# Kernel optimization log

Measured on AMD Instinct MI355X. Metric: run time of the kernel, lower is better.

Reference implementation:

```python
import jax, jax.numpy as jnp
import numpy as np

WAVE_LEN = 1000.0
DIM_G = 64


def box_relational_embedding(boxes):
    # boxes: (B, N, 4) -> (B, N, N, 64) trigonometric geometry embedding
    B, N, _ = boxes.shape
    x_min, y_min, x_max, y_max = jnp.split(boxes, 4, axis=-1)  # each (B,N,1)
    cx = (x_min + x_max) * 0.5
    cy = (y_min + y_max) * 0.5
    w = (x_max - x_min) + 1.0
    h = (y_max - y_min) + 1.0
    cxT = jnp.swapaxes(cx, 1, 2)  # (B,1,N)
    cyT = jnp.swapaxes(cy, 1, 2)
    dx = jnp.log(jnp.clip(jnp.abs((cx - cxT) / w), 1e-3))  # (B,N,N)
    dy = jnp.log(jnp.clip(jnp.abs((cy - cyT) / h), 1e-3))
    dw = jnp.log(w / jnp.swapaxes(w, 1, 2))
    dh = jnp.log(h / jnp.swapaxes(h, 1, 2))
    pos = jnp.stack([dx, dy, dw, dh], axis=-1)  # (B,N,N,4)
    n_freq = DIM_G // 8  # 8 frequency bands
    dim_mat = 1.0 / (WAVE_LEN ** (jnp.arange(n_freq, dtype=pos.dtype) / n_freq))
    mul = (100.0 * pos)[..., None] * dim_mat  # (B,N,N,4,8)
    mul = mul.reshape(B, N, N, 4 * n_freq)  # (B,N,N,32)
    return jnp.concatenate([jnp.sin(mul), jnp.cos(mul)], axis=-1)  # (B,N,N,64)


def setup_inputs() -> dict:
    key = jax.random.key(0)
    ks = jax.random.split(key, 12)
    B, N, D, H = 32, 196, 1024, 8
    scale = 0.02
    inp = {
        "input_query": jax.random.normal(ks[0], (B, N, D), jnp.float32),
        "input_key": jax.random.normal(ks[1], (B, N, D), jnp.float32),
        "input_value": jax.random.normal(ks[2], (B, N, D), jnp.float32),
        "input_box": jax.random.uniform(ks[3], (B, N, 4), jnp.float32),
        "Wq": jax.random.normal(ks[4], (D, D), jnp.float32) * scale,
        "bq": jnp.zeros((D,), jnp.float32),
        "Wk": jax.random.normal(ks[5], (D, D), jnp.float32) * scale,
        "bk": jnp.zeros((D,), jnp.float32),
        "Wv": jax.random.normal(ks[6], (D, D), jnp.float32) * scale,
        "bv": jnp.zeros((D,), jnp.float32),
        "Wo": jax.random.normal(ks[7], (D, D), jnp.float32) * scale,
        "bo": jnp.zeros((D,), jnp.float32),
        "WG_w": jax.random.normal(ks[8], (H, DIM_G), jnp.float32) * scale,  # 8 stacked (64->1) linears
        "WG_b": jnp.zeros((H,), jnp.float32),
    }
    return inp


def reference(input_query, input_key, input_value, input_box,
              Wq, bq, Wk, bk, Wv, bv, Wo, bo, WG_w, WG_b):
    B, N, D = input_query.shape
    H = WG_w.shape[0]
    dk = D // H
    # relation geometry weights per head: (B,H,N,N)
    geo = box_relational_embedding(input_box)  # (B,N,N,64)
    wg = jax.nn.relu(jnp.einsum('bnmg,hg->bhnm', geo, WG_w) + WG_b[None, :, None, None])
    # projections (torch Linear: x @ W.T + b), reshape to (B,H,N,dk)
    def proj(x, W, b):
        return (x @ W.T + b).reshape(B, N, H, dk).transpose(0, 2, 1, 3)
    q = proj(input_query, Wq, bq)
    k = proj(input_key, Wk, bk)
    v = proj(input_value, Wv, bv)
    scores = jnp.einsum('bhnd,bhmd->bhnm', q, k) / np.sqrt(dk).astype(q.dtype)
    logits = jnp.log(jnp.clip(wg, 1e-6)) + scores
    attn = jax.nn.softmax(logits, axis=-1)  # (B,H,N,N)
    out = jnp.einsum('bhnm,bhmd->bhnd', attn, v)  # (B,H,N,dk)
    out = out.transpose(0, 2, 1, 3).reshape(B, N, D)
    return out @ Wo.T + bo
```

## Files before the change

kernel.cpp:

```cpp
#include <hip/hip_runtime.h>
#include <hip/hip_bf16.h>

typedef __bf16 bf16;
typedef _Float16 half_t;
typedef bf16 bf16x8 __attribute__((ext_vector_type(8)));
typedef bf16 bf16x4 __attribute__((ext_vector_type(4)));
typedef float floatx4 __attribute__((ext_vector_type(4)));

#define B_ 32
#define N_ 196
#define H_ 8
#define D_ 1024
#define DK_ 128
#define BN_ (B_ * N_)
#define BH_ (B_ * H_)
#define NPAD_ 224
#define PSTRIDE_ 232

typedef __attribute__((address_space(3))) unsigned int lds_uint;
typedef const __attribute__((address_space(1))) unsigned int glb_uint;

__device__ __forceinline__ void async_copy16(const bf16* g, bf16* l) {
  __builtin_amdgcn_global_load_lds((glb_uint*)g, (lds_uint*)l, 16, 0, 0);
}

__device__ __forceinline__ bf16x8 bzero8() {
  bf16x8 z;
#pragma unroll
  for (int i = 0; i < 8; i++) z[i] = (bf16)0.0f;
  return z;
}

__global__ __launch_bounds__(256) void cvt3_kernel(const float* __restrict__ s0,
                                                   const float* __restrict__ s1,
                                                   const float* __restrict__ s2,
                                                   bf16* __restrict__ d0,
                                                   bf16* __restrict__ d1,
                                                   bf16* __restrict__ d2, int n4) {
  const int which = blockIdx.y;
  const float* s = (which == 0) ? s0 : (which == 1) ? s1 : s2;
  bf16* d = (which == 0) ? d0 : (which == 1) ? d1 : d2;
  int i = blockIdx.x * 256 + threadIdx.x;
  if (i >= n4) return;
  float4 v = ((const float4*)s)[i];
  bf16x4 o;
  o[0] = (bf16)v.x;
  o[1] = (bf16)v.y;
  o[2] = (bf16)v.z;
  o[3] = (bf16)v.w;
  *(bf16x4*)(d + (size_t)i * 4) = o;
}

__global__ __launch_bounds__(256) void cvt4_kernel(const float* __restrict__ s0,
                                                   const float* __restrict__ s1,
                                                   const float* __restrict__ s2,
                                                   const float* __restrict__ s3,
                                                   bf16* __restrict__ d0,
                                                   bf16* __restrict__ d1,
                                                   bf16* __restrict__ d2,
                                                   bf16* __restrict__ d3, int n4) {
  const int which = blockIdx.y;
  const float* s = (which == 0) ? s0 : (which == 1) ? s1 : (which == 2) ? s2 : s3;
  bf16* d = (which == 0) ? d0 : (which == 1) ? d1 : (which == 2) ? d2 : d3;
  int i = blockIdx.x * 256 + threadIdx.x;
  if (i >= n4) return;
  float4 v = ((const float4*)s)[i];
  bf16x4 o;
  o[0] = (bf16)v.x;
  o[1] = (bf16)v.y;
  o[2] = (bf16)v.z;
  o[3] = (bf16)v.w;
  *(bf16x4*)(d + (size_t)i * 4) = o;
}

__global__ __launch_bounds__(256) void geo_kernel(const float* __restrict__ box,
                                                  const float* __restrict__ WGw,
                                                  const float* __restrict__ WGb,
                                                  half_t* __restrict__ S) {
  __shared__ float4 wsh[128];
  if (threadIdx.x < 128) wsh[threadIdx.x] = ((const float4*)WGw)[threadIdx.x];
  __syncthreads();

  int tid = blockIdx.x * 256 + threadIdx.x;
  int b = tid / (N_ * N_);
  int rem = tid - b * (N_ * N_);
  int n = rem / N_;
  int m = rem - n * N_;

  float4 bn = ((const float4*)box)[b * N_ + n];
  float4 bm = ((const float4*)box)[b * N_ + m];
  float cxn = (bn.x + bn.z) * 0.5f, cyn = (bn.y + bn.w) * 0.5f;
  float wn = bn.z - bn.x + 1.0f, hn = bn.w - bn.y + 1.0f;
  float cxm = (bm.x + bm.z) * 0.5f, cym = (bm.y + bm.w) * 0.5f;
  float wm = bm.z - bm.x + 1.0f, hm = bm.w - bm.y + 1.0f;

  float pos[4];
  pos[0] = __logf(fmaxf(fabsf((cxn - cxm) / wn), 1e-3f));
  pos[1] = __logf(fmaxf(fabsf((cyn - cym) / hn), 1e-3f));
  pos[2] = __logf(wn / wm);
  pos[3] = __logf(hn / hm);

  const float dims[8] = {1.0f,          0.4216965034f, 0.1778279410f, 0.0749894209f,
                         0.0316227766f, 0.0133352143f, 0.0056234133f, 0.0023713737f};
  float feat[64];
#pragma unroll
  for (int p = 0; p < 4; p++) {
#pragma unroll
    for (int f = 0; f < 8; f++) {
      float a = 100.0f * pos[p] * dims[f];
      feat[p * 8 + f] = __sinf(a);
      feat[32 + p * 8 + f] = __cosf(a);
    }
  }
#pragma unroll
  for (int hh = 0; hh < 8; hh++) {
    float accv = WGb[hh];
#pragma unroll
    for (int g4 = 0; g4 < 16; g4++) {
      float4 wv = wsh[hh * 16 + g4];
      accv += feat[g4 * 4 + 0] * wv.x + feat[g4 * 4 + 1] * wv.y +
              feat[g4 * 4 + 2] * wv.z + feat[g4 * 4 + 3] * wv.w;
    }
    S[((size_t)((b * H_ + hh) * N_ + n)) * NPAD_ + m] = (half_t)fmaxf(accv, 1e-6f);
  }
}

template <int MODE>
__global__ __launch_bounds__(256) void gemm_nt(const bf16* __restrict__ A,
                                               const bf16* __restrict__ W,
                                               const float* __restrict__ bias,
                                               void* __restrict__ Cout, int M, int K,
                                               int Nd) {
  __shared__ bf16 As[128 * 32];
  __shared__ bf16 Bs[128 * 32];

  const int wave = threadIdx.x >> 6;
  const int lane = threadIdx.x & 63;
  const int l16 = lane & 15;
  const int quad = lane >> 4;

  const bf16* gA = A + (size_t)blockIdx.x * 128 * K;
  const bf16* gB = W + (size_t)blockIdx.y * 128 * K;

  const int srow = lane >> 2;
  const int scol = (lane & 3) * 8;
  const int seg0 = wave * 2;
  const size_t gOffA0 = (size_t)(seg0 * 16 + srow) * K + scol;
  const size_t gOffA1 = (size_t)(seg0 * 16 + 16 + srow) * K + scol;
  bf16* lA0 = As + seg0 * 512 + lane * 8;
  bf16* lA1 = As + (seg0 + 1) * 512 + lane * 8;
  bf16* lB0 = Bs + seg0 * 512 + lane * 8;
  bf16* lB1 = Bs + (seg0 + 1) * 512 + lane * 8;

  floatx4 acc[4][4];
#pragma unroll
  for (int i = 0; i < 4; i++)
#pragma unroll
    for (int j = 0; j < 4; j++)
#pragma unroll
      for (int r = 0; r < 4; r++) acc[i][j][r] = 0.0f;

  async_copy16(gA + gOffA0, lA0);
  async_copy16(gA + gOffA1, lA1);
  async_copy16(gB + gOffA0, lB0);
  async_copy16(gB + gOffA1, lB1);

  const bf16* rA = As + ((wave >> 1) * 64 + l16) * 32 + quad * 8;
  const bf16* rB = Bs + ((wave & 1) * 64 + l16) * 32 + quad * 8;

  for (int k0 = 0; k0 < K; k0 += 32) {
    __syncthreads();
    bf16x8 af[4], bfv[4];
#pragma unroll
    for (int i = 0; i < 4; i++) af[i] = *(const bf16x8*)(rA + i * 16 * 32);
#pragma unroll
    for (int j = 0; j < 4; j++) bfv[j] = *(const bf16x8*)(rB + j * 16 * 32);
    __syncthreads();
    if (k0 + 32 < K) {
      const bf16* gAn = gA + k0 + 32;
      const bf16* gBn = gB + k0 + 32;
      async_copy16(gAn + gOffA0, lA0);
      async_copy16(gAn + gOffA1, lA1);
      async_copy16(gBn + gOffA0, lB0);
      async_copy16(gBn + gOffA1, lB1);
    }
#pragma unroll
    for (int i = 0; i < 4; i++)
#pragma unroll
      for (int j = 0; j < 4; j++)
        acc[i][j] = __builtin_amdgcn_mfma_f32_16x16x32_bf16(af[i], bfv[j], acc[i][j], 0, 0, 0);
  }

  const int m0 = blockIdx.x * 128 + (wave >> 1) * 64;
  const int n0 = blockIdx.y * 128 + (wave & 1) * 64;
#pragma unroll
  for (int j = 0; j < 4; j++) {
    const int col = n0 + j * 16 + l16;
    const float bv = bias[col];
#pragma unroll
    for (int i = 0; i < 4; i++) {
#pragma unroll
      for (int r = 0; r < 4; r++) {
        const int row = m0 + i * 16 + quad * 4 + r;
        float v = acc[i][j][r] + bv;
        if (MODE == 0) {
          ((bf16*)Cout)[(size_t)row * Nd + col] = (bf16)v;
        } else if (MODE == 1) {
          ((float*)Cout)[(size_t)row * Nd + col] = v;
        } else {
          int b = row / N_;
          int n = row - b * N_;
          int h = col >> 7;
          int d = col & (DK_ - 1);
          ((bf16*)Cout)[((size_t)((b * H_ + h) * DK_ + d)) * NPAD_ + n] = (bf16)v;
        }
      }
    }
  }
}

__global__ __launch_bounds__(256) void gemm_qkv(
    const bf16* __restrict__ Aq, const bf16* __restrict__ Ak, const bf16* __restrict__ Av,
    const bf16* __restrict__ Wq, const bf16* __restrict__ Wk, const bf16* __restrict__ Wv,
    const float* __restrict__ bq, const float* __restrict__ bk, const float* __restrict__ bv,
    bf16* __restrict__ Oq, bf16* __restrict__ Ok, bf16* __restrict__ Vt) {
  const int z = blockIdx.z;
  const bf16* A = (z == 0) ? Aq : (z == 1) ? Ak : Av;
  const bf16* W = (z == 0) ? Wq : (z == 1) ? Wk : Wv;
  const float* bias = (z == 0) ? bq : (z == 1) ? bk : bv;
  constexpr int K = D_;

  __shared__ bf16 As[128 * 32];
  __shared__ bf16 Bs[128 * 32];

  const int wave = threadIdx.x >> 6;
  const int lane = threadIdx.x & 63;
  const int l16 = lane & 15;
  const int quad = lane >> 4;

  const bf16* gA = A + (size_t)blockIdx.x * 128 * K;
  const bf16* gB = W + (size_t)blockIdx.y * 128 * K;

  const int srow = lane >> 2;
  const int scol = (lane & 3) * 8;
  const int seg0 = wave * 2;
  const size_t gOffA0 = (size_t)(seg0 * 16 + srow) * K + scol;
  const size_t gOffA1 = (size_t)(seg0 * 16 + 16 + srow) * K + scol;
  bf16* lA0 = As + seg0 * 512 + lane * 8;
  bf16* lA1 = As + (seg0 + 1) * 512 + lane * 8;
  bf16* lB0 = Bs + seg0 * 512 + lane * 8;
  bf16* lB1 = Bs + (seg0 + 1) * 512 + lane * 8;

  floatx4 acc[4][4];
#pragma unroll
  for (int i = 0; i < 4; i++)
#pragma unroll
    for (int j = 0; j < 4; j++)
#pragma unroll
      for (int r = 0; r < 4; r++) acc[i][j][r] = 0.0f;

  async_copy16(gA + gOffA0, lA0);
  async_copy16(gA + gOffA1, lA1);
  async_copy16(gB + gOffA0, lB0);
  async_copy16(gB + gOffA1, lB1);

  const bf16* rA = As + ((wave >> 1) * 64 + l16) * 32 + quad * 8;
  const bf16* rB = Bs + ((wave & 1) * 64 + l16) * 32 + quad * 8;

  for (int k0 = 0; k0 < K; k0 += 32) {
    __syncthreads();
    bf16x8 af[4], bfv[4];
#pragma unroll
    for (int i = 0; i < 4; i++) af[i] = *(const bf16x8*)(rA + i * 16 * 32);
#pragma unroll
    for (int j = 0; j < 4; j++) bfv[j] = *(const bf16x8*)(rB + j * 16 * 32);
    __syncthreads();
    if (k0 + 32 < K) {
      const bf16* gAn = gA + k0 + 32;
      const bf16* gBn = gB + k0 + 32;
      async_copy16(gAn + gOffA0, lA0);
      async_copy16(gAn + gOffA1, lA1);
      async_copy16(gBn + gOffA0, lB0);
      async_copy16(gBn + gOffA1, lB1);
    }
#pragma unroll
    for (int i = 0; i < 4; i++)
#pragma unroll
      for (int j = 0; j < 4; j++)
        acc[i][j] = __builtin_amdgcn_mfma_f32_16x16x32_bf16(af[i], bfv[j], acc[i][j], 0, 0, 0);
  }

  const int m0 = blockIdx.x * 128 + (wave >> 1) * 64;
  const int n0 = blockIdx.y * 128 + (wave & 1) * 64;
  if (z < 2) {
    bf16* Cout = z ? Ok : Oq;
#pragma unroll
    for (int j = 0; j < 4; j++) {
      const int col = n0 + j * 16 + l16;
      const float bv = bias[col];
#pragma unroll
      for (int i = 0; i < 4; i++) {
#pragma unroll
        for (int r = 0; r < 4; r++) {
          const int row = m0 + i * 16 + quad * 4 + r;
          Cout[(size_t)row * D_ + col] = (bf16)(acc[i][j][r] + bv);
        }
      }
    }
  } else {
#pragma unroll
    for (int j = 0; j < 4; j++) {
      const int col = n0 + j * 16 + l16;
      const float bv = bias[col];
      const int h = col >> 7;
      const int d = col & (DK_ - 1);
#pragma unroll
      for (int i = 0; i < 4; i++) {
#pragma unroll
        for (int r = 0; r < 4; r++) {
          const int row = m0 + i * 16 + quad * 4 + r;
          int b = row / N_;
          int n = row - b * N_;
          Vt[((size_t)((b * H_ + h) * DK_ + d)) * NPAD_ + n] = (bf16)(acc[i][j][r] + bv);
        }
      }
    }
  }
}

__global__ __launch_bounds__(256) void attn_kernel(const bf16* __restrict__ Q,
                                                   const bf16* __restrict__ Kmat,
                                                   const bf16* __restrict__ Vt,
                                                   const half_t* __restrict__ Sb,
                                                   bf16* __restrict__ AO) {
  __shared__ bf16 Pl[4 * 16 * PSTRIDE_];

  const int f = blockIdx.x;
  const int tile = (f >> 3) & 3;
  const int bh = (f & 7) | ((f >> 5) << 3);
  const int b = bh >> 3;
  const int h = bh & 7;
  const int wave = threadIdx.x >> 6;
  const int lane = threadIdx.x & 63;
  const int l16 = lane & 15;
  const int quad = lane >> 4;
  const int nrb = tile * 64 + wave * 16;

  floatx4 S[14];
#pragma unroll
  for (int j = 0; j < 14; j++)
#pragma unroll
    for (int r = 0; r < 4; r++) S[j][r] = 0.0f;

  const int na = nrb + l16;
  const bool nav = na < N_;
  const bf16* aptr = Q + ((size_t)(b * N_ + (nav ? na : 0))) * D_ + h * DK_ + quad * 8;
  bf16x8 afr[4];
#pragma unroll
  for (int kk = 0; kk < 4; kk++) afr[kk] = nav ? *(const bf16x8*)(aptr + kk * 32) : bzero8();

#pragma unroll
  for (int j = 0; j < 14; j++) {
    const int m = j * 16 + l16;
    const bool mv = m < N_;
    const bf16* kp = Kmat + ((size_t)(b * N_ + (mv ? m : 0))) * D_ + h * DK_ + quad * 8;
#pragma unroll
    for (int kk = 0; kk < 4; kk++) {
      bf16x8 bb = mv ? *(const bf16x8*)(kp + kk * 32) : bzero8();
      S[j] = __builtin_amdgcn_mfma_f32_16x16x32_bf16(afr[kk], bb, S[j], 0, 0, 0);
    }
  }

  const float scale = 0.08838834764831845f;
  const half_t* bbase = Sb + ((size_t)bh * N_) * NPAD_;
  bf16* pw = Pl + wave * 16 * PSTRIDE_;
  float inv[4];
#pragma unroll
  for (int r = 0; r < 4; r++) {
    const int n = nrb + quad * 4 + r;
    const size_t brow = (size_t)(n < N_ ? n : 0) * NPAD_;
    float mx = S[0][r] * scale;
#pragma unroll
    for (int j = 0; j < 14; j++) {
      S[j][r] *= scale;
      mx = fmaxf(mx, S[j][r]);
    }
#pragma unroll
    for (int off = 1; off < 16; off <<= 1) mx = fmaxf(mx, __shfl_xor(mx, off, 64));
    float sum = 0.0f;
#pragma unroll
    for (int j = 0; j < 14; j++) {
      const int m = j * 16 + l16;
      float w = (m < N_) ? (float)bbase[brow + m] : 0.0f;
      float e = w * __expf(S[j][r] - mx);
      sum += e;
      pw[(quad * 4 + r) * PSTRIDE_ + m] = (bf16)e;
    }
#pragma unroll
    for (int off = 1; off < 16; off <<= 1) sum += __shfl_xor(sum, off, 64);
    inv[r] = 1.0f / sum;
  }
  __syncthreads();

  floatx4 O[8];
#pragma unroll
  for (int j2 = 0; j2 < 8; j2++)
#pragma unroll
    for (int r = 0; r < 4; r++) O[j2][r] = 0.0f;

  const bf16* vbase = Vt + (size_t)bh * DK_ * NPAD_ + quad * 8;
  const bf16* pr = pw + l16 * PSTRIDE_ + quad * 8;
#pragma unroll
  for (int k0 = 0; k0 < NPAD_; k0 += 32) {
    bf16x8 a = *(const bf16x8*)(pr + k0);
#pragma unroll
    for (int j2 = 0; j2 < 8; j2++) {
      bf16x8 bb = *(const bf16x8*)(vbase + (size_t)(j2 * 16 + l16) * NPAD_ + k0);
      O[j2] = __builtin_amdgcn_mfma_f32_16x16x32_bf16(a, bb, O[j2], 0, 0, 0);
    }
  }

#pragma unroll
  for (int r = 0; r < 4; r++) {
    const int n = nrb + quad * 4 + r;
    if (n < N_) {
#pragma unroll
      for (int j2 = 0; j2 < 8; j2++) {
        AO[((size_t)(b * N_ + n)) * D_ + h * DK_ + j2 * 16 + l16] = (bf16)(O[j2][r] * inv[r]);
      }
    }
  }
}

extern "C" void kernel_launch(void* const* d_in, const int* in_sizes, int n_in,
                              void* d_out, int out_size, void* d_ws, size_t ws_size,
                              hipStream_t stream) {
  const float* xq = (const float*)d_in[0];
  const float* xk = (const float*)d_in[1];
  const float* xv = (const float*)d_in[2];
  const float* box = (const float*)d_in[3];
  const float* Wq = (const float*)d_in[4];
  const float* bq = (const float*)d_in[5];
  const float* Wk = (const float*)d_in[6];
  const float* bk = (const float*)d_in[7];
  const float* Wv = (const float*)d_in[8];
  const float* bv = (const float*)d_in[9];
  const float* Wo = (const float*)d_in[10];
  const float* bo = (const float*)d_in[11];
  const float* WGw = (const float*)d_in[12];
  const float* WGb = (const float*)d_in[13];

  size_t off = 0;
  char* wsc = (char*)d_ws;
  auto alloc = [&](size_t bytes) -> void* {
    void* p = wsc + off;
    off += (bytes + 255) & ~(size_t)255;
    return p;
  };
  bf16* xq_b = (bf16*)alloc((size_t)BN_ * D_ * 2);
  bf16* xk_b = (bf16*)alloc((size_t)BN_ * D_ * 2);
  bf16* xv_b = (bf16*)alloc((size_t)BN_ * D_ * 2);
  bf16* wq_b = (bf16*)alloc((size_t)D_ * D_ * 2);
  bf16* wk_b = (bf16*)alloc((size_t)D_ * D_ * 2);
  bf16* wv_b = (bf16*)alloc((size_t)D_ * D_ * 2);
  bf16* wo_b = (bf16*)alloc((size_t)D_ * D_ * 2);
  bf16* q_b = (bf16*)alloc((size_t)BN_ * D_ * 2);
  bf16* k_b = (bf16*)alloc((size_t)BN_ * D_ * 2);
  bf16* vt_b = (bf16*)alloc((size_t)BH_ * DK_ * NPAD_ * 2);
  bf16* ao_b = (bf16*)alloc((size_t)BN_ * D_ * 2);
  half_t* S = (half_t*)alloc((size_t)BH_ * N_ * NPAD_ * 2);

  const int n4x = BN_ * D_ / 4;
  const int n4w = D_ * D_ / 4;
  dim3 g3(n4x / 256, 3, 1);
  cvt3_kernel<<<g3, 256, 0, stream>>>(xq, xk, xv, xq_b, xk_b, xv_b, n4x);
  dim3 g4(n4w / 256, 4, 1);
  cvt4_kernel<<<g4, 256, 0, stream>>>(Wq, Wk, Wv, Wo, wq_b, wk_b, wv_b, wo_b, n4w);

  geo_kernel<<<(B_ * N_ * N_) / 256, 256, 0, stream>>>(box, WGw, WGb, S);

  hipMemsetAsync(vt_b, 0, (size_t)BH_ * DK_ * NPAD_ * 2, stream);

  dim3 gqkv(BN_ / 128, D_ / 128, 3);
  gemm_qkv<<<gqkv, 256, 0, stream>>>(xq_b, xk_b, xv_b, wq_b, wk_b, wv_b, bq, bk, bv,
                                     q_b, k_b, vt_b);

  attn_kernel<<<1024, 256, 0, stream>>>(q_b, k_b, vt_b, S, ao_b);

  dim3 gproj(BN_ / 128, D_ / 128, 1);
  gemm_nt<1><<<gproj, 256, 0, stream>>>(ao_b, wo_b, bo, d_out, BN_, D_, D_);
}
```

Before: 369.8 us.

## Replace projection GEMMs with 8-wave 128x256 triple-buffered swizzled LDS pipeline

Replaces the two separate 128x128 GEMM kernels with one templated 512-thread kernel that computes 128x256 output tiles with K-step 64. The kernel keeps three LDS stages, prefetching two steps ahead with async global-to-LDS copies. It uses an XOR swizzle on LDS slots to avoid bank conflicts and interleaves MFMA phases with the prefetch issues under explicit waitcnt/barrier and setprio. This targets the memory-latency-bound single-buffer loop of the old GEMMs. In exchange it uses about 144KB of LDS, so only one block fits per CU, and 49x4x3 blocks may tail unevenly across the CUs.

```diff
diff --git a/kernel.cpp b/kernel.cpp
--- a/kernel.cpp
+++ b/kernel.cpp
@@ -17,6 +17,10 @@
 #define NPAD_ 224
 #define PSTRIDE_ 232
 
+#define MT_ 49
+#define NTILE_ 4
+#define KT_ 16
+
 typedef __attribute__((address_space(3))) unsigned int lds_uint;
 typedef const __attribute__((address_space(1))) unsigned int glb_uint;
 
@@ -30,6 +34,10 @@
   for (int i = 0; i < 8; i++) z[i] = (bf16)0.0f;
   return z;
 }
+
+#define BARRIER() asm volatile("s_barrier" ::: "memory")
+#define WAITV6() asm volatile("s_waitcnt vmcnt(6)" ::: "memory")
+#define WAITV0() asm volatile("s_waitcnt vmcnt(0)" ::: "memory")
 
 __global__ __launch_bounds__(256) void cvt3_kernel(const float* __restrict__ s0,
                                                    const float* __restrict__ s1,
@@ -125,32 +133,45 @@
   }
 }
 
-template <int MODE>
-__global__ __launch_bounds__(256) void gemm_nt(const bf16* __restrict__ A,
-                                               const bf16* __restrict__ W,
-                                               const float* __restrict__ bias,
-                                               void* __restrict__ Cout, int M, int K,
-                                               int Nd) {
-  __shared__ bf16 As[128 * 32];
-  __shared__ bf16 Bs[128 * 32];
-
-  const int wave = threadIdx.x >> 6;
-  const int lane = threadIdx.x & 63;
+template <int VARIANT>
+__global__ __launch_bounds__(512, 1) void gemm8p(
+    const bf16* __restrict__ A0, const bf16* __restrict__ A1, const bf16* __restrict__ A2,
+    const bf16* __restrict__ W0, const bf16* __restrict__ W1, const bf16* __restrict__ W2,
+    const float* __restrict__ b0, const float* __restrict__ b1, const float* __restrict__ b2,
+    void* __restrict__ O0, void* __restrict__ O1, void* __restrict__ O2) {
+  __shared__ bf16 Asb[3][128 * 64];
+  __shared__ bf16 Bsb[3][256 * 64];
+
+  const int z = (VARIANT == 0) ? blockIdx.z : 0;
+  const bf16* A = (z == 0) ? A0 : (z == 1) ? A1 : A2;
+  const bf16* W = (z == 0) ? W0 : (z == 1) ? W1 : W2;
+  const float* bias = (z == 0) ? b0 : (z == 1) ? b1 : b2;
+
+  const int tid = threadIdx.x;
+  const int lane = tid & 63;
+  const int wid = tid >> 6;
   const int l16 = lane & 15;
   const int quad = lane >> 4;
-
-  const bf16* gA = A + (size_t)blockIdx.x * 128 * K;
-  const bf16* gB = W + (size_t)blockIdx.y * 128 * K;
-
-  const int srow = lane >> 2;
-  const int scol = (lane & 3) * 8;
-  const int seg0 = wave * 2;
-  const size_t gOffA0 = (size_t)(seg0 * 16 + srow) * K + scol;
-  const size_t gOffA1 = (size_t)(seg0 * 16 + 16 + srow) * K + scol;
-  bf16* lA0 = As + seg0 * 512 + lane * 8;
-  bf16* lA1 = As + (seg0 + 1) * 512 + lane * 8;
-  bf16* lB0 = Bs + seg0 * 512 + lane * 8;
-  bf16* lB1 = Bs + (seg0 + 1) * 512 + lane * 8;
+  const int wm = wid >> 2;
+  const int wn = wid & 3;
+
+  const bf16* gA = A + (size_t)blockIdx.y * 128 * D_;
+  const bf16* gB = W + (size_t)blockIdx.x * 256 * D_;
+
+  const int srow = tid >> 3;
+  const int lslot = (tid & 7) ^ (srow & 7);
+  const size_t s0 = (size_t)srow * D_ + lslot * 8;
+  const size_t s1 = (size_t)(64 + srow) * D_ + lslot * 8;
+  const size_t s2 = (size_t)(128 + srow) * D_ + lslot * 8;
+  const size_t s3 = (size_t)(192 + srow) * D_ + lslot * 8;
+
+  int arow[4], brow[4], kslot[2];
+#pragma unroll
+  for (int i = 0; i < 4; i++) arow[i] = (wm * 64 + i * 16 + l16) * 64;
+#pragma unroll
+  for (int j = 0; j < 4; j++) brow[j] = (wn * 64 + j * 16 + l16) * 64;
+#pragma unroll
+  for (int kk = 0; kk < 2; kk++) kslot[kk] = (((kk * 4 + quad) ^ (l16 & 7)) * 8);
 
   floatx4 acc[4][4];
 #pragma unroll
@@ -160,39 +181,78 @@
 #pragma unroll
       for (int r = 0; r < 4; r++) acc[i][j][r] = 0.0f;
 
-  async_copy16(gA + gOffA0, lA0);
-  async_copy16(gA + gOffA1, lA1);
-  async_copy16(gB + gOffA0, lB0);
-  async_copy16(gB + gOffA1, lB1);
-
-  const bf16* rA = As + ((wave >> 1) * 64 + l16) * 32 + quad * 8;
-  const bf16* rB = Bs + ((wave & 1) * 64 + l16) * 32 + quad * 8;
-
-  for (int k0 = 0; k0 < K; k0 += 32) {
-    __syncthreads();
-    bf16x8 af[4], bfv[4];
-#pragma unroll
-    for (int i = 0; i < 4; i++) af[i] = *(const bf16x8*)(rA + i * 16 * 32);
-#pragma unroll
-    for (int j = 0; j < 4; j++) bfv[j] = *(const bf16x8*)(rB + j * 16 * 32);
-    __syncthreads();
-    if (k0 + 32 < K) {
-      const bf16* gAn = gA + k0 + 32;
-      const bf16* gBn = gB + k0 + 32;
-      async_copy16(gAn + gOffA0, lA0);
-      async_copy16(gAn + gOffA1, lA1);
-      async_copy16(gBn + gOffA0, lB0);
-      async_copy16(gBn + gOffA1, lB1);
-    }
-#pragma unroll
-    for (int i = 0; i < 4; i++)
-#pragma unroll
-      for (int j = 0; j < 4; j++)
-        acc[i][j] = __builtin_amdgcn_mfma_f32_16x16x32_bf16(af[i], bfv[j], acc[i][j], 0, 0, 0);
-  }
-
-  const int m0 = blockIdx.x * 128 + (wave >> 1) * 64;
-  const int n0 = blockIdx.y * 128 + (wave & 1) * 64;
+#pragma unroll
+  for (int kt = 0; kt < 2; kt++) {
+    const bf16* sa = gA + kt * 64;
+    const bf16* sb = gB + kt * 64;
+    async_copy16(sa + s0, &Asb[kt][tid * 8]);
+    async_copy16(sa + s1, &Asb[kt][4096 + tid * 8]);
+    async_copy16(sb + s0, &Bsb[kt][tid * 8]);
+    async_copy16(sb + s1, &Bsb[kt][4096 + tid * 8]);
+    async_copy16(sb + s2, &Bsb[kt][8192 + tid * 8]);
+    async_copy16(sb + s3, &Bsb[kt][12288 + tid * 8]);
+  }
+  WAITV6();
+  BARRIER();
+
+  for (int kt = 0; kt < KT_; ++kt) {
+    const int g = kt % 3;
+    const int gn = (kt + 2) % 3;
+    const bool pf = (kt + 2 < KT_);
+    const bf16* Ab = Asb[g];
+    const bf16* Bb = Bsb[g];
+    const bf16* pa = gA + (kt + 2) * 64;
+    const bf16* pb = gB + (kt + 2) * 64;
+    bf16x8 af[2][2], bfv[2][2];
+#pragma unroll
+    for (int ph = 0; ph < 4; ++ph) {
+      const int ih = ph >> 1;
+      const int jh = ph & 1;
+      if (jh == 0) {
+#pragma unroll
+        for (int i2 = 0; i2 < 2; i2++)
+#pragma unroll
+          for (int kk = 0; kk < 2; kk++)
+            af[i2][kk] = *(const bf16x8*)(Ab + arow[2 * ih + i2] + kslot[kk]);
+      }
+#pragma unroll
+      for (int j2 = 0; j2 < 2; j2++)
+#pragma unroll
+        for (int kk = 0; kk < 2; kk++)
+          bfv[j2][kk] = *(const bf16x8*)(Bb + brow[2 * jh + j2] + kslot[kk]);
+      if (pf) {
+        if (ph == 0) {
+          async_copy16(pa + s0, &Asb[gn][tid * 8]);
+          async_copy16(pa + s1, &Asb[gn][4096 + tid * 8]);
+        } else if (ph == 1) {
+          async_copy16(pb + s0, &Bsb[gn][tid * 8]);
+          async_copy16(pb + s1, &Bsb[gn][4096 + tid * 8]);
+        } else if (ph == 2) {
+          async_copy16(pb + s2, &Bsb[gn][8192 + tid * 8]);
+          async_copy16(pb + s3, &Bsb[gn][12288 + tid * 8]);
+        }
+      }
+      BARRIER();
+      __builtin_amdgcn_s_setprio(1);
+#pragma unroll
+      for (int i2 = 0; i2 < 2; i2++)
+#pragma unroll
+        for (int j2 = 0; j2 < 2; j2++)
+#pragma unroll
+          for (int kk = 0; kk < 2; kk++)
+            acc[2 * ih + i2][2 * jh + j2] = __builtin_amdgcn_mfma_f32_16x16x32_bf16(
+                af[i2][kk], bfv[j2][kk], acc[2 * ih + i2][2 * jh + j2], 0, 0, 0);
+      __builtin_amdgcn_s_setprio(0);
+      if (ph == 3 && kt < KT_ - 1) {
+        if (pf) WAITV6();
+        else    WAITV0();
+      }
+      BARRIER();
+    }
+  }
+
+  const int m0 = blockIdx.y * 128 + wm * 64;
+  const int n0 = blockIdx.x * 256 + wn * 64;
 #pragma unroll
   for (int j = 0; j < 4; j++) {
     const int col = n0 + j * 16 + l16;
@@ -203,125 +263,17 @@
       for (int r = 0; r < 4; r++) {
         const int row = m0 + i * 16 + quad * 4 + r;
         float v = acc[i][j][r] + bv;
-        if (MODE == 0) {
-          ((bf16*)Cout)[(size_t)row * Nd + col] = (bf16)v;
-        } else if (MODE == 1) {
-          ((float*)Cout)[(size_t)row * Nd + col] = v;
+        if (VARIANT == 1) {
+          ((float*)O0)[(size_t)row * D_ + col] = v;
+        } else if (z < 2) {
+          bf16* Cout = z ? (bf16*)O1 : (bf16*)O0;
+          Cout[(size_t)row * D_ + col] = (bf16)v;
         } else {
           int b = row / N_;
           int n = row - b * N_;
           int h = col >> 7;
           int d = col & (DK_ - 1);
-          ((bf16*)Cout)[((size_t)((b * H_ + h) * DK_ + d)) * NPAD_ + n] = (bf16)v;
-        }
-      }
-    }
-  }
-}
-
-__global__ __launch_bounds__(256) void gemm_qkv(
-    const bf16* __restrict__ Aq, const bf16* __restrict__ Ak, const bf16* __restrict__ Av,
-    const bf16* __restrict__ Wq, const bf16* __restrict__ Wk, const bf16* __restrict__ Wv,
-    const float* __restrict__ bq, const float* __restrict__ bk, const float* __restrict__ bv,
-    bf16* __restrict__ Oq, bf16* __restrict__ Ok, bf16* __restrict__ Vt) {
-  const int z = blockIdx.z;
-  const bf16* A = (z == 0) ? Aq : (z == 1) ? Ak : Av;
-  const bf16* W = (z == 0) ? Wq : (z == 1) ? Wk : Wv;
-  const float* bias = (z == 0) ? bq : (z == 1) ? bk : bv;
-  constexpr int K = D_;
-
-  __shared__ bf16 As[128 * 32];
-  __shared__ bf16 Bs[128 * 32];
-
-  const int wave = threadIdx.x >> 6;
-  const int lane = threadIdx.x & 63;
-  const int l16 = lane & 15;
-  const int quad = lane >> 4;
-
-  const bf16* gA = A + (size_t)blockIdx.x * 128 * K;
-  const bf16* gB = W + (size_t)blockIdx.y * 128 * K;
-
-  const int srow = lane >> 2;
-  const int scol = (lane & 3) * 8;
-  const int seg0 = wave * 2;
-  const size_t gOffA0 = (size_t)(seg0 * 16 + srow) * K + scol;
-  const size_t gOffA1 = (size_t)(seg0 * 16 + 16 + srow) * K + scol;
-  bf16* lA0 = As + seg0 * 512 + lane * 8;
-  bf16* lA1 = As + (seg0 + 1) * 512 + lane * 8;
-  bf16* lB0 = Bs + seg0 * 512 + lane * 8;
-  bf16* lB1 = Bs + (seg0 + 1) * 512 + lane * 8;
-
-  floatx4 acc[4][4];
-#pragma unroll
-  for (int i = 0; i < 4; i++)
-#pragma unroll
-    for (int j = 0; j < 4; j++)
-#pragma unroll
-      for (int r = 0; r < 4; r++) acc[i][j][r] = 0.0f;
-
-  async_copy16(gA + gOffA0, lA0);
-  async_copy16(gA + gOffA1, lA1);
-  async_copy16(gB + gOffA0, lB0);
-  async_copy16(gB + gOffA1, lB1);
-
-  const bf16* rA = As + ((wave >> 1) * 64 + l16) * 32 + quad * 8;
-  const bf16* rB = Bs + ((wave & 1) * 64 + l16) * 32 + quad * 8;
-
-  for (int k0 = 0; k0 < K; k0 += 32) {
-    __syncthreads();
-    bf16x8 af[4], bfv[4];
-#pragma unroll
-    for (int i = 0; i < 4; i++) af[i] = *(const bf16x8*)(rA + i * 16 * 32);
-#pragma unroll
-    for (int j = 0; j < 4; j++) bfv[j] = *(const bf16x8*)(rB + j * 16 * 32);
-    __syncthreads();
-    if (k0 + 32 < K) {
-      const bf16* gAn = gA + k0 + 32;
-      const bf16* gBn = gB + k0 + 32;
-      async_copy16(gAn + gOffA0, lA0);
-      async_copy16(gAn + gOffA1, lA1);
-      async_copy16(gBn + gOffA0, lB0);
-      async_copy16(gBn + gOffA1, lB1);
-    }
-#pragma unroll
-    for (int i = 0; i < 4; i++)
-#pragma unroll
-      for (int j = 0; j < 4; j++)
-        acc[i][j] = __builtin_amdgcn_mfma_f32_16x16x32_bf16(af[i], bfv[j], acc[i][j], 0, 0, 0);
-  }
-
-  const int m0 = blockIdx.x * 128 + (wave >> 1) * 64;
-  const int n0 = blockIdx.y * 128 + (wave & 1) * 64;
-  if (z < 2) {
-    bf16* Cout = z ? Ok : Oq;
-#pragma unroll
-    for (int j = 0; j < 4; j++) {
-      const int col = n0 + j * 16 + l16;
-      const float bv = bias[col];
-#pragma unroll
-      for (int i = 0; i < 4; i++) {
-#pragma unroll
-        for (int r = 0; r < 4; r++) {
-          const int row = m0 + i * 16 + quad * 4 + r;
-          Cout[(size_t)row * D_ + col] = (bf16)(acc[i][j][r] + bv);
-        }
-      }
-    }
-  } else {
-#pragma unroll
-    for (int j = 0; j < 4; j++) {
-      const int col = n0 + j * 16 + l16;
-      const float bv = bias[col];
-      const int h = col >> 7;
-      const int d = col & (DK_ - 1);
-#pragma unroll
-      for (int i = 0; i < 4; i++) {
-#pragma unroll
-        for (int r = 0; r < 4; r++) {
-          const int row = m0 + i * 16 + quad * 4 + r;
-          int b = row / N_;
-          int n = row - b * N_;
-          Vt[((size_t)((b * H_ + h) * DK_ + d)) * NPAD_ + n] = (bf16)(acc[i][j][r] + bv);
+          ((bf16*)O2)[((size_t)((b * H_ + h) * DK_ + d)) * NPAD_ + n] = (bf16)v;
         }
       }
     }
@@ -481,12 +433,13 @@
 
   hipMemsetAsync(vt_b, 0, (size_t)BH_ * DK_ * NPAD_ * 2, stream);
 
-  dim3 gqkv(BN_ / 128, D_ / 128, 3);
-  gemm_qkv<<<gqkv, 256, 0, stream>>>(xq_b, xk_b, xv_b, wq_b, wk_b, wv_b, bq, bk, bv,
-                                     q_b, k_b, vt_b);
+  dim3 gqkv(NTILE_, MT_, 3);
+  gemm8p<0><<<gqkv, 512, 0, stream>>>(xq_b, xk_b, xv_b, wq_b, wk_b, wv_b, bq, bk, bv,
+                                      q_b, k_b, vt_b);
 
   attn_kernel<<<1024, 256, 0, stream>>>(q_b, k_b, vt_b, S, ao_b);
 
-  dim3 gproj(BN_ / 128, D_ / 128, 1);
-  gemm_nt<1><<<gproj, 256, 0, stream>>>(ao_b, wo_b, bo, d_out, BN_, D_, D_);
-}
+  dim3 gout(NTILE_, MT_, 1);
+  gemm8p<1><<<gout, 512, 0, stream>>>(ao_b, nullptr, nullptr, wo_b, nullptr, nullptr,
+                                      bo, nullptr, nullptr, d_out, nullptr, nullptr);
+}
```

Result: no change. 370.2 us (+0.1%).
